# Kernel tuning notes

Hardware: AMD Instinct MI355X
Metric: run time of the kernel (lower is better)

Reference implementation:

```python
import jax, jax.numpy as jnp
import numpy as np

N, C, H, W = 16, 512, 64, 64
C_BAR, C_HAT = 64, 256


def max_pool2(t):
    # t: [n, c, h, w] -> [n, c, h//2, w//2] via 2x2 max pool
    n, c, h, w = t.shape
    return t.reshape(n, c, h // 2, 2, w // 2, 2).max(axis=(3, 5))


def setup_inputs() -> dict:
    key = jax.random.key(0)
    ks = jax.random.split(key, 6)
    x = jax.random.normal(ks[0], (N, C, H, W), dtype=jnp.float32)
    # 1x1 conv weights stored as [out_channels, in_channels]
    w_theta = jax.random.normal(ks[1], (C_BAR, C), dtype=jnp.float32) * 0.02
    w_phi = jax.random.normal(ks[2], (C_BAR, C), dtype=jnp.float32) * 0.02
    w_g = jax.random.normal(ks[3], (C_HAT, C), dtype=jnp.float32) * 0.02
    w_o = jax.random.normal(ks[4], (C, C_HAT), dtype=jnp.float32) * 0.02
    # gamma initialized to zero in the module; use a small nonzero value so the
    # attention path contributes to the output (and to gradients).
    gamma = jnp.full((1,), 0.1, dtype=jnp.float32)
    return {"x": x, "w_theta": w_theta, "w_phi": w_phi, "w_g": w_g,
            "w_o": w_o, "gamma": gamma}


def reference(x, w_theta, w_phi, w_g, w_o, gamma):
    n, c, h, w = x.shape
    hw, hw4 = h * w, (h * w) // 4
    # 1x1 conv projections (pure channel GEMMs)
    g_x = jnp.einsum('nchw,oc->nohw', x, w_g)          # [n, c_hat, h, w]
    g_x = max_pool2(g_x).reshape(n, -1, hw4)            # [n, c_hat, hw/4]
    phi_x = jnp.einsum('nchw,oc->nohw', x, w_phi)       # [n, c_bar, h, w]
    phi_x = max_pool2(phi_x).reshape(n, -1, hw4)        # [n, c_bar, hw/4]
    theta_x = jnp.einsum('nchw,oc->nohw', x, w_theta).reshape(n, -1, hw)  # [n, c_bar, hw]
    # bmm -> softmax -> bmm
    scores = jnp.einsum('nds,ndt->nst', theta_x, phi_x)  # [n, hw, hw/4]
    attn = jax.nn.softmax(scores, axis=-1)
    y = jnp.einsum('ndt,nst->nds', g_x, attn)            # [n, c_hat, hw]
    y = y.reshape(n, -1, h, w)
    o = jnp.einsum('nchw,oc->nohw', y, w_o)              # [n, c, h, w]
    return gamma[0] * o + x
```

## Files before the change

kernel.cpp:

```cpp
#include <hip/hip_runtime.h>
#include <stdint.h>

typedef unsigned short u16;
typedef u16   us4 __attribute__((ext_vector_type(4)));
typedef u16   us8 __attribute__((ext_vector_type(8)));
typedef __bf16 bf8 __attribute__((ext_vector_type(8)));
typedef float f4  __attribute__((ext_vector_type(4)));

__device__ __forceinline__ u16 f2bf(float f) {
    uint32_t u = __builtin_bit_cast(uint32_t, f);
    uint32_t r = (u + 0x7fffu + ((u >> 16) & 1u)) >> 16;
    return (u16)r;
}
__device__ __forceinline__ float bf2f(u16 s) {
    uint32_t u = ((uint32_t)s) << 16;
    return __builtin_bit_cast(float, u);
}
__device__ __forceinline__ f4 mfma16(bf8 a, bf8 b, f4 c) {
    return __builtin_amdgcn_mfma_f32_16x16x32_bf16(a, b, c, 0, 0, 0);
}
__device__ __forceinline__ u16 max4bf(u16 a, u16 b, u16 c, u16 d) {
    float m = fmaxf(fmaxf(bf2f(a), bf2f(b)), fmaxf(bf2f(c), bf2f(d)));
    return f2bf(m);
}

__global__ __launch_bounds__(256) void xt_kernel(
    const float* __restrict__ x, u16* __restrict__ Xt)
{
    const int s0 = blockIdx.x * 64, c0 = blockIdx.y * 64, n = blockIdx.z;
    const int tid = threadIdx.x;
    __shared__ u16 lds[64 * 72];

    {
        int c_loc = tid & 63, s_seg = (tid >> 6) * 16;
        const float* src = x + ((size_t)n * 512 + c0 + c_loc) * 4096 + s0 + s_seg;
        for (int i4 = 0; i4 < 4; i4++) {
            float4 f = *(const float4*)(src + i4 * 4);
            int s = s_seg + i4 * 4;
            lds[(s + 0) * 72 + c_loc] = f2bf(f.x);
            lds[(s + 1) * 72 + c_loc] = f2bf(f.y);
            lds[(s + 2) * 72 + c_loc] = f2bf(f.z);
            lds[(s + 3) * 72 + c_loc] = f2bf(f.w);
        }
    }
    __syncthreads();
    {
        int s_loc = tid >> 2, c_seg = (tid & 3) * 16;
        u16* dst = Xt + ((size_t)n * 4096 + s0 + s_loc) * 512 + c0 + c_seg;
        *(us8*)(dst)     = *(const us8*)&lds[s_loc * 72 + c_seg];
        *(us8*)(dst + 8) = *(const us8*)&lds[s_loc * 72 + c_seg + 8];
    }
}

__global__ __launch_bounds__(256) void wconv_kernel(
    const float* __restrict__ w_theta, const float* __restrict__ w_phi,
    const float* __restrict__ w_g, const float* __restrict__ w_o,
    u16* __restrict__ Wall_bf, u16* __restrict__ Wo_bf)
{
    int base = (blockIdx.x * 256 + threadIdx.x) * 4;
    const float* src; u16* dst;
    if (base < 32768)       { src = w_theta + base;          dst = Wall_bf + base; }
    else if (base < 65536)  { src = w_phi + (base - 32768);  dst = Wall_bf + base; }
    else if (base < 196608) { src = w_g + (base - 65536);    dst = Wall_bf + base; }
    else                    { src = w_o + (base - 196608);   dst = Wo_bf + (base - 196608); }
    float4 f = *(const float4*)src;
    us4 v; v[0] = f2bf(f.x); v[1] = f2bf(f.y); v[2] = f2bf(f.z); v[3] = f2bf(f.w);
    *(us4*)dst = v;
}

__global__ __launch_bounds__(256) void projT_gemm(
    const u16* __restrict__ Xt, const u16* __restrict__ Wall_bf,
    u16* __restrict__ PT)
{
    const int s0 = blockIdx.x * 128;
    const int r0 = blockIdx.y * 128;
    const int nb = blockIdx.z;
    const int tid = threadIdx.x;
    const int wave = tid >> 6, lane = tid & 63;
    const int quad = lane >> 4, l15 = lane & 15;
    const int wm = (wave >> 1) * 64, wn = (wave & 1) * 64;

    __shared__ u16 a_lds[128 * 40];
    __shared__ u16 b_lds[128 * 40];

    f4 acc[4][4];
    f4 z = {0.f, 0.f, 0.f, 0.f};
    for (int i = 0; i < 4; i++) for (int j = 0; j < 4; j++) acc[i][j] = z;

    const u16* Abase = Xt + ((size_t)nb * 4096 + s0) * 512;
    const int m = tid >> 1, kseg = (tid & 1) * 16;

    for (int k0 = 0; k0 < 512; k0 += 32) {
        *(us8*)&a_lds[m * 40 + kseg]     = *(const us8*)(Abase + (size_t)m * 512 + k0 + kseg);
        *(us8*)&a_lds[m * 40 + kseg + 8] = *(const us8*)(Abase + (size_t)m * 512 + k0 + kseg + 8);
        *(us8*)&b_lds[m * 40 + kseg]     = *(const us8*)(Wall_bf + (size_t)(r0 + m) * 512 + k0 + kseg);
        *(us8*)&b_lds[m * 40 + kseg + 8] = *(const us8*)(Wall_bf + (size_t)(r0 + m) * 512 + k0 + kseg + 8);
        __syncthreads();
        bf8 af[4], bfr[4];
        for (int i = 0; i < 4; i++)
            af[i]  = __builtin_bit_cast(bf8, *(const us8*)&a_lds[(wm + i*16 + l15)*40 + quad*8]);
        for (int j = 0; j < 4; j++)
            bfr[j] = __builtin_bit_cast(bf8, *(const us8*)&b_lds[(wn + j*16 + l15)*40 + quad*8]);
        for (int i = 0; i < 4; i++)
            for (int j = 0; j < 4; j++)
                acc[i][j] = mfma16(af[i], bfr[j], acc[i][j]);
        __syncthreads();
    }
    for (int i = 0; i < 4; i++) {
        int s_idx = s0 + wm + i * 16 + quad * 4;
        for (int rr = 0; rr < 4; rr++) {
            u16* dst = PT + ((size_t)nb * 4096 + s_idx + rr) * 384 + r0 + wn + l15;
            for (int j = 0; j < 4; j++)
                dst[j * 16] = f2bf(acc[i][j][rr]);
        }
    }
}

__global__ __launch_bounds__(256) void phi_pool2(
    const u16* __restrict__ PT, u16* __restrict__ phiF)
{
    int n = blockIdx.y, t0 = blockIdx.x * 64;
    int tid = threadIdx.x;
    int t_loc = tid >> 2, d0 = (tid & 3) * 16;
    int t = t0 + t_loc;
    int h2 = t >> 5, w2 = t & 31;
    int s00 = h2 * 128 + w2 * 2;
    const u16* base = PT + ((size_t)n * 4096) * 384 + 64 + d0;
    us8 r[4][2];
    int soff[4] = {s00, s00 + 1, s00 + 64, s00 + 65};
    for (int p = 0; p < 4; p++) {
        r[p][0] = *(const us8*)(base + (size_t)soff[p] * 384);
        r[p][1] = *(const us8*)(base + (size_t)soff[p] * 384 + 8);
    }
    us8 o0, o1;
    for (int i = 0; i < 8; i++) {
        o0[i] = max4bf(r[0][0][i], r[1][0][i], r[2][0][i], r[3][0][i]);
        o1[i] = max4bf(r[0][1][i], r[1][1][i], r[2][1][i], r[3][1][i]);
    }
    size_t fb = (((size_t)n * 32 + (t >> 5)) * 2 + ((t >> 4) & 1)) * 1024
              + (size_t)(d0 >> 5) * 512
              + (size_t)(((d0 >> 3) & 3) * 16 + (t & 15)) * 8;
    *(us8*)(phiF + fb)       = o0;
    *(us8*)(phiF + fb + 128) = o1;
}

__global__ __launch_bounds__(256) void g_poolT(
    const u16* __restrict__ PT, u16* __restrict__ gF)
{
    int t0 = blockIdx.x * 64, d0 = blockIdx.y * 64, n = blockIdx.z;
    int tid = threadIdx.x;
    __shared__ u16 lds[64 * 72];

    {
        int t_loc = tid & 63, dseg = (tid >> 6) * 16;
        int t = t0 + t_loc;
        int h2 = t >> 5, w2 = t & 31;
        int s00 = h2 * 128 + w2 * 2;
        const u16* base = PT + ((size_t)n * 4096) * 384 + 128 + d0 + dseg;
        us8 r[4][2];
        int soff[4] = {s00, s00 + 1, s00 + 64, s00 + 65};
        for (int p = 0; p < 4; p++) {
            r[p][0] = *(const us8*)(base + (size_t)soff[p] * 384);
            r[p][1] = *(const us8*)(base + (size_t)soff[p] * 384 + 8);
        }
        for (int i = 0; i < 8; i++) {
            lds[(dseg + i) * 72 + t_loc]     = max4bf(r[0][0][i], r[1][0][i], r[2][0][i], r[3][0][i]);
            lds[(dseg + 8 + i) * 72 + t_loc] = max4bf(r[0][1][i], r[1][1][i], r[2][1][i], r[3][1][i]);
        }
    }
    __syncthreads();
    {
        int d_loc = tid >> 2, t_seg = (tid & 3) * 16;
        size_t fb = ((((size_t)n * 4 + blockIdx.y) * 4 + (d_loc >> 4)) * 32
                     + (t0 >> 5) + (t_seg >> 5)) * 512
                  + (size_t)((((t_seg >> 3) & 3)) * 16 + (d_loc & 15)) * 8;
        *(us8*)(gF + fb)       = *(const us8*)&lds[d_loc * 72 + t_seg];
        *(us8*)(gF + fb + 128) = *(const us8*)&lds[d_loc * 72 + t_seg + 8];
    }
}

__global__ __launch_bounds__(256) void attn_kernel(
    const u16* __restrict__ PT, const u16* __restrict__ phiF,
    const u16* __restrict__ gF, u16* __restrict__ yT)
{
    const int orig = blockIdx.x;
    const int tile = (orig & 7) * 128 + (orig >> 3);
    const int n = tile >> 6;
    const int q0b = (tile & 63) * 64;

    const int tid = threadIdx.x;
    const int wave = tid >> 6, lane = tid & 63, quad = lane >> 4, l15 = lane & 15;

    __shared__ u16 p_lds[2][4][16 * 40];
    __shared__ float qsum[64];

    const u16* th = PT + ((size_t)n * 4096 + q0b + wave * 16 + l15) * 384 + quad * 8;
    bf8 bth0 = __builtin_bit_cast(bf8, *(const us8*)(th));
    bf8 bth1 = __builtin_bit_cast(bf8, *(const us8*)(th + 32));

    const u16* pbase = phiF + (size_t)n * 65536 + lane * 8;
    const u16* gbase = gF + ((size_t)n * 4 + wave) * 65536 + lane * 8;

    f4 z = {0.f, 0.f, 0.f, 0.f};
    f4 acc[4][4];
    for (int i = 0; i < 4; i++) for (int j = 0; j < 4; j++) acc[i][j] = z;
    float lsum = 0.f;

    us8 ph00 = *(const us8*)(pbase);
    us8 ph01 = *(const us8*)(pbase + 512);
    us8 ph10 = *(const us8*)(pbase + 1024);
    us8 ph11 = *(const us8*)(pbase + 1536);
    us8 gg0 = *(const us8*)(gbase);
    us8 gg1 = *(const us8*)(gbase + 16384);
    us8 gg2 = *(const us8*)(gbase + 32768);
    us8 gg3 = *(const us8*)(gbase + 49152);

    for (int ci = 0; ci < 32; ci++) {
        const int buf = ci & 1;
        {
            f4 s = mfma16(__builtin_bit_cast(bf8, ph00), bth0, z);
            s = mfma16(__builtin_bit_cast(bf8, ph01), bth1, s);
            us4 pk; float ps = 0.f;
            for (int rr = 0; rr < 4; rr++) { float p = __expf(s[rr]); ps += p; pk[rr] = f2bf(p); }
            lsum += ps;
            *(us4*)&p_lds[buf][wave][l15 * 40 + quad * 4] = pk;
        }
        {
            f4 s = mfma16(__builtin_bit_cast(bf8, ph10), bth0, z);
            s = mfma16(__builtin_bit_cast(bf8, ph11), bth1, s);
            us4 pk; float ps = 0.f;
            for (int rr = 0; rr < 4; rr++) { float p = __expf(s[rr]); ps += p; pk[rr] = f2bf(p); }
            lsum += ps;
            *(us4*)&p_lds[buf][wave][l15 * 40 + 16 + quad * 4] = pk;
        }

        __syncthreads();

        bf8 ag0 = __builtin_bit_cast(bf8, gg0);
        bf8 ag1 = __builtin_bit_cast(bf8, gg1);
        bf8 ag2 = __builtin_bit_cast(bf8, gg2);
        bf8 ag3 = __builtin_bit_cast(bf8, gg3);
        {
            const int nc = (ci + 1 < 32) ? ci + 1 : 31;
            const u16* pb = pbase + (size_t)nc * 2048;
            ph00 = *(const us8*)(pb);
            ph01 = *(const us8*)(pb + 512);
            ph10 = *(const us8*)(pb + 1024);
            ph11 = *(const us8*)(pb + 1536);
            const u16* gb = gbase + (size_t)nc * 512;
            gg0 = *(const us8*)(gb);
            gg1 = *(const us8*)(gb + 16384);
            gg2 = *(const us8*)(gb + 32768);
            gg3 = *(const us8*)(gb + 49152);
        }

        for (int j = 0; j < 4; j++) {
            bf8 bp = __builtin_bit_cast(bf8, *(const us8*)&p_lds[buf][j][l15 * 40 + quad * 8]);
            acc[0][j] = mfma16(ag0, bp, acc[0][j]);
            acc[1][j] = mfma16(ag1, bp, acc[1][j]);
            acc[2][j] = mfma16(ag2, bp, acc[2][j]);
            acc[3][j] = mfma16(ag3, bp, acc[3][j]);
        }
    }

    float v = lsum;
    v += __shfl_xor(v, 16);
    v += __shfl_xor(v, 32);
    if (lane < 16) qsum[wave * 16 + lane] = v;
    __syncthreads();

    for (int j = 0; j < 4; j++) {
        float invj = 1.0f / qsum[j * 16 + l15];
        u16* dst = yT + ((size_t)n * 4096 + q0b + j * 16 + l15) * 256 + wave * 64 + quad * 4;
        for (int i = 0; i < 4; i++) {
            us4 o;
            for (int rr = 0; rr < 4; rr++) o[rr] = f2bf(acc[i][j][rr] * invj);
            *(us4*)(dst + i * 16) = o;
        }
    }
}

__global__ __launch_bounds__(256) void oproj_gemm(
    const u16* __restrict__ Wo_bf, const u16* __restrict__ yT,
    const float* __restrict__ x, const float* __restrict__ gamma,
    float* __restrict__ out)
{
    const int nt = blockIdx.x;
    const int mt = blockIdx.y;
    const int nb = blockIdx.z;
    const int tid = threadIdx.x;
    const int wave = tid >> 6, lane = tid & 63;
    const int quad = lane >> 4, l15 = lane & 15;
    const int wm = (wave >> 1) * 32, wn = (wave & 1) * 64;
    const int s0 = nt * 128;

    __shared__ u16 a_lds[64 * 40];
    __shared__ u16 b_lds[128 * 40];

    f4 acc[2][4];
    f4 z = {0.f, 0.f, 0.f, 0.f};
    for (int i = 0; i < 2; i++) for (int j = 0; j < 4; j++) acc[i][j] = z;

    for (int k0 = 0; k0 < 256; k0 += 32) {
        {
            int m = tid >> 2, kq = (tid & 3) * 8;
            *(us8*)&a_lds[m * 40 + kq] =
                *(const us8*)(Wo_bf + (size_t)(mt * 64 + m) * 256 + k0 + kq);
        }
        {
            int s_loc = tid >> 1, kq = (tid & 1) * 16;
            const u16* src = yT + ((size_t)nb * 4096 + s0 + s_loc) * 256 + k0 + kq;
            *(us8*)&b_lds[s_loc * 40 + kq]     = *(const us8*)(src);
            *(us8*)&b_lds[s_loc * 40 + kq + 8] = *(const us8*)(src + 8);
        }
        __syncthreads();
        bf8 af[2], bfr[4];
        for (int i = 0; i < 2; i++)
            af[i] = __builtin_bit_cast(bf8, *(const us8*)&a_lds[(wm + i*16 + l15)*40 + quad*8]);
        for (int j = 0; j < 4; j++)
            bfr[j] = __builtin_bit_cast(bf8, *(const us8*)&b_lds[(wn + j*16 + l15)*40 + quad*8]);
        for (int i = 0; i < 2; i++)
            for (int j = 0; j < 4; j++)
                acc[i][j] = mfma16(af[i], bfr[j], acc[i][j]);
        __syncthreads();
    }
    float g0 = gamma[0];
    for (int i = 0; i < 2; i++) {
        int c = mt * 64 + wm + i * 16 + quad * 4;
        for (int j = 0; j < 4; j++) {
            int s = s0 + wn + j * 16 + l15;
            for (int rr = 0; rr < 4; rr++) {
                size_t idx = ((size_t)nb * 512 + c + rr) * 4096 + s;
                out[idx] = g0 * acc[i][j][rr] + x[idx];
            }
        }
    }
}

extern "C" void kernel_launch(void* const* d_in, const int* in_sizes, int n_in,
                              void* d_out, int out_size, void* d_ws, size_t ws_size,
                              hipStream_t stream)
{
    (void)in_sizes; (void)n_in; (void)out_size; (void)ws_size;
    const float* x       = (const float*)d_in[0];
    const float* w_theta = (const float*)d_in[1];
    const float* w_phi   = (const float*)d_in[2];
    const float* w_g     = (const float*)d_in[3];
    const float* w_o     = (const float*)d_in[4];
    const float* gamma   = (const float*)d_in[5];
    float* out = (float*)d_out;

    char* ws = (char*)d_ws;
    u16* Xt      = (u16*)(ws);
    u16* yT      = (u16*)(ws);
    u16* phiF    = (u16*)(ws + 33554432);
    u16* gF      = (u16*)(ws + 35651584);
    u16* Wall_bf = (u16*)(ws + 67108864);
    u16* Wo_bf   = (u16*)(ws + 67502080);
    u16* PT      = (u16*)(ws + 67764224);

    xt_kernel  <<<dim3(64, 8, 16), 256, 0, stream>>>(x, Xt);
    wconv_kernel<<<320, 256, 0, stream>>>(w_theta, w_phi, w_g, w_o, Wall_bf, Wo_bf);
    projT_gemm <<<dim3(32, 3, 16), 256, 0, stream>>>(Xt, Wall_bf, PT);
    phi_pool2  <<<dim3(16, 16),    256, 0, stream>>>(PT, phiF);
    g_poolT    <<<dim3(16, 4, 16), 256, 0, stream>>>(PT, gF);
    attn_kernel<<<dim3(1024),      256, 0, stream>>>(PT, phiF, gF, yT);
    oproj_gemm <<<dim3(32, 8, 16), 256, 0, stream>>>(Wo_bf, yT, x, gamma, out);
}
```

Measured before the change: 419.4 us.

## Widen attention tiles to 128 queries with shared LDS-staged phi

```diff
diff --git a/kernel.cpp b/kernel.cpp
--- a/kernel.cpp
+++ b/kernel.cpp
@@ -15,6 +15,9 @@
 __device__ __forceinline__ float bf2f(u16 s) {
     uint32_t u = ((uint32_t)s) << 16;
     return __builtin_bit_cast(float, u);
+}
+__device__ __forceinline__ u16 cvtbf(float f) {
+    return __builtin_bit_cast(u16, (__bf16)f);
 }
 __device__ __forceinline__ f4 mfma16(bf8 a, bf8 b, f4 c) {
     return __builtin_amdgcn_mfma_f32_16x16x32_bf16(a, b, c, 0, 0, 0);
@@ -179,88 +182,91 @@
     }
 }
 
-__global__ __launch_bounds__(256) void attn_kernel(
+__global__ __launch_bounds__(512, 4) void attn_kernel(
     const u16* __restrict__ PT, const u16* __restrict__ phiF,
     const u16* __restrict__ gF, u16* __restrict__ yT)
 {
     const int orig = blockIdx.x;
-    const int tile = (orig & 7) * 128 + (orig >> 3);
-    const int n = tile >> 6;
-    const int q0b = (tile & 63) * 64;
+    const int tile = (orig & 7) * 64 + (orig >> 3);
+    const int n = tile >> 5;
+    const int q0b = (tile & 31) * 128;
 
     const int tid = threadIdx.x;
     const int wave = tid >> 6, lane = tid & 63, quad = lane >> 4, l15 = lane & 15;
 
-    __shared__ u16 p_lds[2][4][16 * 40];
-    __shared__ float qsum[64];
+    __shared__ u16 p_lds[2][8][16 * 40];
+    __shared__ u16 phi_lds[2][32 * 72];
+    __shared__ float qsum[128];
 
     const u16* th = PT + ((size_t)n * 4096 + q0b + wave * 16 + l15) * 384 + quad * 8;
     bf8 bth0 = __builtin_bit_cast(bf8, *(const us8*)(th));
     bf8 bth1 = __builtin_bit_cast(bf8, *(const us8*)(th + 32));
 
-    const u16* pbase = phiF + (size_t)n * 65536 + lane * 8;
-    const u16* gbase = gF + ((size_t)n * 4 + wave) * 65536 + lane * 8;
+    const u16* gbase = gF + ((size_t)n * 16 + wave * 2) * 16384 + lane * 8;
+
+    const u16* phi_src = phiF + (size_t)n * 65536 + tid * 4;
+    const int sl = (tid >> 1) & 63;
+    const int st = ((tid >> 8) & 1) * 16 + (sl & 15);
+    const int sd = ((tid >> 7) & 1) * 32 + (sl >> 4) * 8 + (tid & 1) * 4;
+    u16* pdst0 = &phi_lds[0][st * 72 + sd];
+    u16* pdst1 = &phi_lds[1][st * 72 + sd];
 
     f4 z = {0.f, 0.f, 0.f, 0.f};
-    f4 acc[4][4];
-    for (int i = 0; i < 4; i++) for (int j = 0; j < 4; j++) acc[i][j] = z;
+    f4 acc[2][8];
+    for (int i = 0; i < 2; i++) for (int j = 0; j < 8; j++) acc[i][j] = z;
     float lsum = 0.f;
 
-    us8 ph00 = *(const us8*)(pbase);
-    us8 ph01 = *(const us8*)(pbase + 512);
-    us8 ph10 = *(const us8*)(pbase + 1024);
-    us8 ph11 = *(const us8*)(pbase + 1536);
+    {
+        us4 p0 = *(const us4*)(phi_src);
+        *(us4*)pdst0 = p0;
+    }
+    us4 pf = *(const us4*)(phi_src + 2048);
     us8 gg0 = *(const us8*)(gbase);
     us8 gg1 = *(const us8*)(gbase + 16384);
-    us8 gg2 = *(const us8*)(gbase + 32768);
-    us8 gg3 = *(const us8*)(gbase + 49152);
+    __syncthreads();
 
     for (int ci = 0; ci < 32; ci++) {
         const int buf = ci & 1;
+        const u16* pl  = buf ? phi_lds[1] : phi_lds[0];
+        u16* pbw = buf ? &p_lds[1][0][0] : &p_lds[0][0][0];
+
+        for (int tt = 0; tt < 2; tt++) {
+            bf8 ap0 = __builtin_bit_cast(bf8, *(const us8*)&pl[(tt * 16 + l15) * 72 + quad * 8]);
+            bf8 ap1 = __builtin_bit_cast(bf8, *(const us8*)&pl[(tt * 16 + l15) * 72 + 32 + quad * 8]);
+            f4 s = mfma16(ap0, bth0, z);
+            s = mfma16(ap1, bth1, s);
+            us4 pk; float ps = 0.f;
+            for (int rr = 0; rr < 4; rr++) {
+                float p = __expf(s[rr]);
+                ps += p;
+                pk[rr] = cvtbf(p);
+            }
+            lsum += ps;
+            *(us4*)&pbw[wave * 640 + l15 * 40 + tt * 16 + quad * 4] = pk;
+        }
+
+        *(us4*)(buf ? pdst0 : pdst1) = pf;
+
+        __syncthreads();
+
+        us8 ggn0, ggn1;
         {
-            f4 s = mfma16(__builtin_bit_cast(bf8, ph00), bth0, z);
-            s = mfma16(__builtin_bit_cast(bf8, ph01), bth1, s);
-            us4 pk; float ps = 0.f;
-            for (int rr = 0; rr < 4; rr++) { float p = __expf(s[rr]); ps += p; pk[rr] = f2bf(p); }
-            lsum += ps;
-            *(us4*)&p_lds[buf][wave][l15 * 40 + quad * 4] = pk;
-        }
-        {
-            f4 s = mfma16(__builtin_bit_cast(bf8, ph10), bth0, z);
-            s = mfma16(__builtin_bit_cast(bf8, ph11), bth1, s);
-            us4 pk; float ps = 0.f;
-            for (int rr = 0; rr < 4; rr++) { float p = __expf(s[rr]); ps += p; pk[rr] = f2bf(p); }
-            lsum += ps;
-            *(us4*)&p_lds[buf][wave][l15 * 40 + 16 + quad * 4] = pk;
-        }
-
-        __syncthreads();
+            const int c2 = (ci + 2 < 32) ? ci + 2 : 31;
+            pf = *(const us4*)(phi_src + (size_t)c2 * 2048);
+            const int c1 = (ci + 1 < 32) ? ci + 1 : 31;
+            ggn0 = *(const us8*)(gbase + (size_t)c1 * 512);
+            ggn1 = *(const us8*)(gbase + 16384 + (size_t)c1 * 512);
+        }
 
         bf8 ag0 = __builtin_bit_cast(bf8, gg0);
         bf8 ag1 = __builtin_bit_cast(bf8, gg1);
-        bf8 ag2 = __builtin_bit_cast(bf8, gg2);
-        bf8 ag3 = __builtin_bit_cast(bf8, gg3);
-        {
-            const int nc = (ci + 1 < 32) ? ci + 1 : 31;
-            const u16* pb = pbase + (size_t)nc * 2048;
-            ph00 = *(const us8*)(pb);
-            ph01 = *(const us8*)(pb + 512);
-            ph10 = *(const us8*)(pb + 1024);
-            ph11 = *(const us8*)(pb + 1536);
-            const u16* gb = gbase + (size_t)nc * 512;
-            gg0 = *(const us8*)(gb);
-            gg1 = *(const us8*)(gb + 16384);
-            gg2 = *(const us8*)(gb + 32768);
-            gg3 = *(const us8*)(gb + 49152);
-        }
-
-        for (int j = 0; j < 4; j++) {
-            bf8 bp = __builtin_bit_cast(bf8, *(const us8*)&p_lds[buf][j][l15 * 40 + quad * 8]);
+        const u16* pbr = buf ? &p_lds[1][0][0] : &p_lds[0][0][0];
+        for (int j = 0; j < 8; j++) {
+            bf8 bp = __builtin_bit_cast(bf8, *(const us8*)&pbr[j * 640 + l15 * 40 + quad * 8]);
             acc[0][j] = mfma16(ag0, bp, acc[0][j]);
             acc[1][j] = mfma16(ag1, bp, acc[1][j]);
-            acc[2][j] = mfma16(ag2, bp, acc[2][j]);
-            acc[3][j] = mfma16(ag3, bp, acc[3][j]);
-        }
+        }
+        gg0 = ggn0; gg1 = ggn1;
     }
 
     float v = lsum;
@@ -269,12 +275,12 @@
     if (lane < 16) qsum[wave * 16 + lane] = v;
     __syncthreads();
 
-    for (int j = 0; j < 4; j++) {
+    for (int j = 0; j < 8; j++) {
         float invj = 1.0f / qsum[j * 16 + l15];
-        u16* dst = yT + ((size_t)n * 4096 + q0b + j * 16 + l15) * 256 + wave * 64 + quad * 4;
-        for (int i = 0; i < 4; i++) {
+        u16* dst = yT + ((size_t)n * 4096 + q0b + j * 16 + l15) * 256 + wave * 32 + quad * 4;
+        for (int i = 0; i < 2; i++) {
             us4 o;
-            for (int rr = 0; rr < 4; rr++) o[rr] = f2bf(acc[i][j][rr] * invj);
+            for (int rr = 0; rr < 4; rr++) o[rr] = cvtbf(acc[i][j][rr] * invj);
             *(us4*)(dst + i * 16) = o;
         }
     }
@@ -364,6 +370,6 @@
     projT_gemm <<<dim3(32, 3, 16), 256, 0, stream>>>(Xt, Wall_bf, PT);
     phi_pool2  <<<dim3(16, 16),    256, 0, stream>>>(PT, phiF);
     g_poolT    <<<dim3(16, 4, 16), 256, 0, stream>>>(PT, gF);
-    attn_kernel<<<dim3(1024),      256, 0, stream>>>(PT, phiF, gF, yT);
+    attn_kernel<<<dim3(512),       512, 0, stream>>>(PT, phiF, gF, yT);
     oproj_gemm <<<dim3(32, 8, 16), 256, 0, stream>>>(Wo_bf, yT, x, gamma, out);
 }
```

Result: faster. 405.2 us (-3.4%).
